# Kernel optimization log

Hardware: AMD Instinct MI355X
Metric: run time of the kernel (lower is better)

Reference implementation:

```python
import jax, jax.numpy as jnp
import numpy as np

V, D, H, B, LK, LQ, PAD = 10000, 300, 512, 16, 64, 64, 0


def _lstm(x, Wih, Whh, b, h0, c0):
    # x: [B,T,D]; Wih: [4G,D]; Whh: [4G,G]; b: [4G] (b_ih+b_hh); torch gate order i,f,g,o
    xg = jnp.einsum('btd,gd->btg', x, Wih) + b
    def step(hc, xt):
        h, c = hc
        g = xt + h @ Whh.T
        i, f, gg, o = jnp.split(g, 4, axis=-1)
        c = jax.nn.sigmoid(f) * c + jax.nn.sigmoid(i) * jnp.tanh(gg)
        h = jax.nn.sigmoid(o) * jnp.tanh(c)
        return (h, c), h
    (hT, cT), hs = jax.lax.scan(step, (h0, c0), jnp.swapaxes(xg, 0, 1))
    return jnp.swapaxes(hs, 0, 1), hT, cT


def setup_inputs() -> dict:
    key = jax.random.key(0)
    ks = jax.random.split(key, 24)
    n = lambda k, s: (jax.random.normal(k, s, jnp.float32) * 0.05)
    return {
        'source': jax.random.randint(ks[0], (B, LK), 0, V),
        'prev_outputs': jax.random.randint(ks[1], (B, LQ), 0, V),
        'emb': n(ks[2], (V, D)),
        'enc_f_Wih': n(ks[3], (4 * H, D)), 'enc_f_Whh': n(ks[4], (4 * H, H)), 'enc_f_b': n(ks[5], (4 * H,)),
        'enc_b_Wih': n(ks[6], (4 * H, D)), 'enc_b_Whh': n(ks[7], (4 * H, H)), 'enc_b_b': n(ks[8], (4 * H,)),
        'dec_Wih': n(ks[9], (8 * H, D)), 'dec_Whh': n(ks[10], (8 * H, 2 * H)), 'dec_b': n(ks[11], (8 * H,)),
        'k_W': n(ks[12], (2 * H, 2 * H)), 'k_b': n(ks[13], (2 * H,)),
        'v_W': n(ks[14], (2 * H, 2 * H)), 'v_b': n(ks[15], (2 * H,)),
        'fc1_W': n(ks[16], (2 * H, 4 * H)), 'fc1_b': n(ks[17], (2 * H,)),
        'fc2_W': n(ks[18], (V, 2 * H)), 'fc2_b': n(ks[19], (V,)),
    }


def reference(source, prev_outputs, emb, enc_f_Wih, enc_f_Whh, enc_f_b,
              enc_b_Wih, enc_b_Whh, enc_b_b, dec_Wih, dec_Whh, dec_b,
              k_W, k_b, v_W, v_b, fc1_W, fc1_b, fc2_W, fc2_b):
    bsz = source.shape[0]
    xs = emb[source]  # [B,LK,300]
    z = jnp.zeros((bsz, H), xs.dtype)
    out_f, hf, cf = _lstm(xs, enc_f_Wih, enc_f_Whh, enc_f_b, z, z)
    out_b, hb, cb = _lstm(xs[:, ::-1], enc_b_Wih, enc_b_Whh, enc_b_b, z, z)
    enc_out = jnp.concatenate([out_f, out_b[:, ::-1]], axis=-1)  # [B,LK,1024]
    # self.change: interleave fwd/bwd channels -> [B,1024]
    h0 = jnp.stack([hf, hb], axis=-1).reshape(bsz, 2 * H)
    c0 = jnp.stack([cf, cb], axis=-1).reshape(bsz, 2 * H)
    Q, _, _ = _lstm(emb[prev_outputs], dec_Wih, dec_Whh, dec_b, h0, c0)  # [B,LQ,1024]
    K = enc_out @ k_W.T + k_b
    Vv = enc_out @ v_W.T + v_b
    M = jnp.einsum('bqc,bkc->bqk', Q, K)
    mask = (source == PAD)[:, None, :]
    M = jnp.where(mask, -jnp.inf, M)
    A = jax.nn.softmax(M, axis=2)
    ctx = jnp.einsum('bqk,bkc->bqc', A, Vv)  # == (A[...,None]*V[:,None]).sum(2)
    x = jnp.tanh(jnp.concatenate([ctx, Q], axis=-1) @ fc1_W.T + fc1_b)  # dropout=identity (eval)
    return x @ fc2_W.T + fc2_b
```

## Files before the change

kernel.cpp:

```cpp
#include <hip/hip_runtime.h>
#include <cmath>

#define BB   16
#define LKK  64
#define LQQ  64
#define DD   300
#define HH   512
#define H2   1024
#define G4   2048
#define G8   4096
#define VV   10000

__device__ __forceinline__ float sigmoidf_(float x) { return 1.f / (1.f + expf(-x)); }

typedef __attribute__((ext_vector_type(4))) float    f4_;
typedef __attribute__((ext_vector_type(4))) unsigned u4_;

__device__ __forceinline__ void st_sc(float* p, float v) {
    __hip_atomic_store(p, v, __ATOMIC_RELAXED, __HIP_MEMORY_SCOPE_AGENT);
}

__device__ __forceinline__ f4_ ld4_sc(const float* p) {
    f4_ r;
    asm volatile("global_load_dwordx4 %0, %1, off sc0 sc1" : "=v"(r) : "v"(p));
    return r;
}
__device__ __forceinline__ u4_ ld4u_sc(const unsigned* p) {
    u4_ r;
    asm volatile("global_load_dwordx4 %0, %1, off sc0 sc1" : "=v"(r) : "v"(p));
    return r;
}
__device__ __forceinline__ void wait_vm0() {
    asm volatile("s_waitcnt vmcnt(0)" ::: "memory");
    __builtin_amdgcn_sched_barrier(0);
}

__device__ __forceinline__ void gbar2(unsigned* flags, int wg, unsigned target) {
    asm volatile("s_waitcnt vmcnt(0)" ::: "memory");
    if (threadIdx.x == 0)
        __hip_atomic_store(&flags[wg], target, __ATOMIC_RELAXED, __HIP_MEMORY_SCOPE_AGENT);
    if (threadIdx.x < 64) {
        for (;;) {
            u4_ f = ld4u_sc(flags + (threadIdx.x << 2));
            wait_vm0();
            unsigned m0 = f[0] < f[1] ? f[0] : f[1];
            unsigned m1 = f[2] < f[3] ? f[2] : f[3];
            unsigned mn = m0 < m1 ? m0 : m1;
            if (__all((int)(mn >= target))) break;
            __builtin_amdgcn_s_sleep(1);
        }
    }
    __syncthreads();
}

__global__ void rev_idx_kernel(const int* __restrict__ src, int* __restrict__ rev,
                               unsigned* __restrict__ bars) {
    int tid = blockIdx.x * blockDim.x + threadIdx.x;
    if (tid < 512) bars[tid] = 0u;
    if (tid < BB * LKK) {
        int b = tid / LKK, t = tid % LKK;
        rev[tid] = src[b * LKK + (LKK - 1 - t)];
    }
}

typedef __attribute__((ext_vector_type(8))) short bfrag8;
typedef __attribute__((ext_vector_type(4))) float facc4;

__device__ __forceinline__ unsigned short f2bf(float x) {
    unsigned u = __float_as_uint(x);
    unsigned r = (u + 0x7fffu + ((u >> 16) & 1u)) >> 16;
    return (unsigned short)r;
}

#define ASTR 40

__device__ __forceinline__ void gemm_core(
        short* __restrict__ Ah, short* __restrict__ Al,
        short* __restrict__ Bh, short* __restrict__ Bl,
        const float* __restrict__ A, const int* __restrict__ gidx, int lda,
        const float* __restrict__ Bw, int ldb,
        const float* __restrict__ bias,
        float* __restrict__ C, int ldc,
        int N, int K, int act, int m0, int n0) {
    int tid = threadIdx.x;
    int lane = tid & 63, w = tid >> 6;
    int wr = w >> 1, wc = w & 1;
    int fr = lane & 15, fg = lane >> 4;

    int sr = tid >> 1, sc = (tid & 1) << 4;
    long abase = gidx ? (long)gidx[m0 + sr] * lda : (long)(m0 + sr) * lda;
    int gn = n0 + sr;
    bool bval = gn < N;
    long bbase = (long)gn * ldb;

    facc4 acc[4][4] = {};

    for (int k0 = 0; k0 < K; k0 += 32) {
        {
            float v[16];
            if (k0 + sc + 16 <= K) {
                const float* ap = A + abase + k0 + sc;
                float4 t0 = *(const float4*)(ap + 0);
                float4 t1 = *(const float4*)(ap + 4);
                float4 t2 = *(const float4*)(ap + 8);
                float4 t3 = *(const float4*)(ap + 12);
                v[0]=t0.x; v[1]=t0.y; v[2]=t0.z;  v[3]=t0.w;
                v[4]=t1.x; v[5]=t1.y; v[6]=t1.z;  v[7]=t1.w;
                v[8]=t2.x; v[9]=t2.y; v[10]=t2.z; v[11]=t2.w;
                v[12]=t3.x; v[13]=t3.y; v[14]=t3.z; v[15]=t3.w;
            } else {
#pragma unroll
                for (int c = 0; c < 16; c++) {
                    int k = k0 + sc + c;
                    v[c] = (k < K) ? A[abase + k] : 0.f;
                }
            }
            bfrag8 h0, h1, l0, l1;
#pragma unroll
            for (int c = 0; c < 8; c++) {
                unsigned short hb = f2bf(v[c]);
                float hf = __uint_as_float(((unsigned)hb) << 16);
                h0[c] = (short)hb; l0[c] = (short)f2bf(v[c] - hf);
            }
#pragma unroll
            for (int c = 0; c < 8; c++) {
                unsigned short hb = f2bf(v[8 + c]);
                float hf = __uint_as_float(((unsigned)hb) << 16);
                h1[c] = (short)hb; l1[c] = (short)f2bf(v[8 + c] - hf);
            }
            *(bfrag8*)&Ah[sr * ASTR + sc]     = h0;
            *(bfrag8*)&Ah[sr * ASTR + sc + 8] = h1;
            *(bfrag8*)&Al[sr * ASTR + sc]     = l0;
            *(bfrag8*)&Al[sr * ASTR + sc + 8] = l1;
        }
        {
            float v[16];
            if (bval && (k0 + sc + 16 <= K)) {
                const float* bp = Bw + bbase + k0 + sc;
                float4 t0 = *(const float4*)(bp + 0);
                float4 t1 = *(const float4*)(bp + 4);
                float4 t2 = *(const float4*)(bp + 8);
                float4 t3 = *(const float4*)(bp + 12);
                v[0]=t0.x; v[1]=t0.y; v[2]=t0.z;  v[3]=t0.w;
                v[4]=t1.x; v[5]=t1.y; v[6]=t1.z;  v[7]=t1.w;
                v[8]=t2.x; v[9]=t2.y; v[10]=t2.z; v[11]=t2.w;
                v[12]=t3.x; v[13]=t3.y; v[14]=t3.z; v[15]=t3.w;
            } else {
#pragma unroll
                for (int c = 0; c < 16; c++) {
                    int k = k0 + sc + c;
                    v[c] = (bval && k < K) ? Bw[bbase + k] : 0.f;
                }
            }
            bfrag8 h0, h1, l0, l1;
#pragma unroll
            for (int c = 0; c < 8; c++) {
                unsigned short hb = f2bf(v[c]);
                float hf = __uint_as_float(((unsigned)hb) << 16);
                h0[c] = (short)hb; l0[c] = (short)f2bf(v[c] - hf);
            }
#pragma unroll
            for (int c = 0; c < 8; c++) {
                unsigned short hb = f2bf(v[8 + c]);
                float hf = __uint_as_float(((unsigned)hb) << 16);
                h1[c] = (short)hb; l1[c] = (short)f2bf(v[8 + c] - hf);
            }
            *(bfrag8*)&Bh[sr * ASTR + sc]     = h0;
            *(bfrag8*)&Bh[sr * ASTR + sc + 8] = h1;
            *(bfrag8*)&Bl[sr * ASTR + sc]     = l0;
            *(bfrag8*)&Bl[sr * ASTR + sc + 8] = l1;
        }
        __syncthreads();

        bfrag8 ah[4], al[4], bh[4], bl[4];
#pragma unroll
        for (int i = 0; i < 4; i++) {
            int ar = wr * 64 + i * 16 + fr;
            ah[i] = *(const bfrag8*)&Ah[ar * ASTR + fg * 8];
            al[i] = *(const bfrag8*)&Al[ar * ASTR + fg * 8];
            int br = wc * 64 + i * 16 + fr;
            bh[i] = *(const bfrag8*)&Bh[br * ASTR + fg * 8];
            bl[i] = *(const bfrag8*)&Bl[br * ASTR + fg * 8];
        }
#pragma unroll
        for (int i = 0; i < 4; i++)
#pragma unroll
            for (int j = 0; j < 4; j++) {
                acc[i][j] = __builtin_amdgcn_mfma_f32_16x16x32_bf16(ah[i], bh[j], acc[i][j], 0, 0, 0);
                acc[i][j] = __builtin_amdgcn_mfma_f32_16x16x32_bf16(ah[i], bl[j], acc[i][j], 0, 0, 0);
                acc[i][j] = __builtin_amdgcn_mfma_f32_16x16x32_bf16(al[i], bh[j], acc[i][j], 0, 0, 0);
            }
        __syncthreads();
    }

#pragma unroll
    for (int i = 0; i < 4; i++) {
        int row = m0 + wr * 64 + i * 16 + fg * 4;
#pragma unroll
        for (int j = 0; j < 4; j++) {
            int col = n0 + wc * 64 + j * 16 + fr;
            if (col < N) {
                float bz = bias[col];
#pragma unroll
                for (int q = 0; q < 4; q++) {
                    float vv = acc[i][j][q] + bz;
                    if (act == 1) vv = tanhf(vv);
                    C[(long)(row + q) * ldc + col] = vv;
                }
            }
        }
    }
}

__global__ __launch_bounds__(256)
void gemm_mfma128(const float* __restrict__ A, const int* __restrict__ gidx, int lda,
                  const float* __restrict__ Bw, int ldb,
                  const float* __restrict__ bias,
                  float* __restrict__ C, int ldc,
                  int N, int K, int act) {
    __shared__ __align__(16) short Ah[128 * ASTR];
    __shared__ __align__(16) short Al[128 * ASTR];
    __shared__ __align__(16) short Bh[128 * ASTR];
    __shared__ __align__(16) short Bl[128 * ASTR];
    gemm_core(Ah, Al, Bh, Bl, A, gidx, lda, Bw, ldb, bias, C, ldc, N, K, act,
              blockIdx.x * 128, blockIdx.y * 128);
}

__global__ __launch_bounds__(256)
void gemm_kv(const float* __restrict__ enc_out,
             const float* __restrict__ kW, const float* __restrict__ kb,
             const float* __restrict__ vW, const float* __restrict__ vb,
             float* __restrict__ Kbuf, float* __restrict__ Vbuf) {
    __shared__ __align__(16) short Ah[128 * ASTR];
    __shared__ __align__(16) short Al[128 * ASTR];
    __shared__ __align__(16) short Bh[128 * ASTR];
    __shared__ __align__(16) short Bl[128 * ASTR];
    int ny = blockIdx.y;
    if (ny < 8)
        gemm_core(Ah, Al, Bh, Bl, enc_out, nullptr, H2, kW, H2, kb, Kbuf, H2,
                  H2, H2, 0, blockIdx.x * 128, ny * 128);
    else
        gemm_core(Ah, Al, Bh, Bl, enc_out, nullptr, H2, vW, H2, vb, Vbuf, H2,
                  H2, H2, 0, blockIdx.x * 128, (ny - 8) * 128);
}

__global__ __launch_bounds__(256)
void gemm_xg(const float* __restrict__ emb,
             const int* __restrict__ src, const int* __restrict__ rev,
             const int* __restrict__ prev,
             const float* __restrict__ Wf, const float* __restrict__ bf,
             const float* __restrict__ Wb, const float* __restrict__ bb,
             const float* __restrict__ Wd, const float* __restrict__ bd,
             float* __restrict__ xf, float* __restrict__ xb,
             float* __restrict__ xd) {
    __shared__ __align__(16) short Ah[128 * ASTR];
    __shared__ __align__(16) short Al[128 * ASTR];
    __shared__ __align__(16) short Bh[128 * ASTR];
    __shared__ __align__(16) short Bl[128 * ASTR];
    int ny = blockIdx.y;
    if (ny < 16)
        gemm_core(Ah, Al, Bh, Bl, emb, src, DD, Wf, DD, bf, xf, G4,
                  G4, DD, 0, blockIdx.x * 128, ny * 128);
    else if (ny < 32)
        gemm_core(Ah, Al, Bh, Bl, emb, rev, DD, Wb, DD, bb, xb, G4,
                  G4, DD, 0, blockIdx.x * 128, (ny - 16) * 128);
    else
        gemm_core(Ah, Al, Bh, Bl, emb, prev, DD, Wd, DD, bd, xd, G8,
                  G8, DD, 0, blockIdx.x * 128, (ny - 32) * 128);
}

__global__ __launch_bounds__(256, 1)
void enc_recur(const float* __restrict__ xg_f, const float* __restrict__ xg_b,
               const float* __restrict__ Wf, const float* __restrict__ Wb,
               float* __restrict__ hglob, float* __restrict__ enc_out,
               float* __restrict__ encc, unsigned* __restrict__ flags) {
    __shared__ float hs[HH * 16];
    __shared__ float red[256 * 33];
    __shared__ float g256[256];
    int wg  = blockIdx.x;
    int dir = wg >> 7;
    int j0  = (wg & 127) * 4;
    int tid = threadIdx.x;
    int ks   = tid & 31;
    int tile = tid >> 5;
    int bh   = tile >> 2;
    int gate = tile & 3;
    int sw   = (ks >> 2) & 3;
    const float* W  = dir ? Wb : Wf;
    const float* xg = dir ? xg_b : xg_f;

    float wreg[4][16];
#pragma unroll
    for (int jn = 0; jn < 4; jn++) {
        const float* wrow = W + (long)(gate * HH + j0 + jn) * HH;
#pragma unroll
        for (int j = 0; j < 16; j++) wreg[jn][j] = wrow[ks + 32 * j];
    }

    int ub = tid & 15, ujj = tid >> 4;
    int xb = tid >> 4, xgate = (tid >> 2) & 3, xjn = tid & 3;
    float creg = 0.f;
    float4* hsv = (float4*)hs;

    for (int t = 0; t < LKK; t++) {
        if (t == 0) {
            for (int i = tid; i < HH * 16; i += 256) hs[i] = 0.f;
        } else {
            const float* hg = hglob + (long)((dir << 1) | (t & 1)) * (HH * 16);
            f4_ vv[8];
#pragma unroll
            for (int u = 0; u < 8; u++) vv[u] = ld4_sc(hg + tid * 4 + u * 1024);
            wait_vm0();
#pragma unroll
            for (int u = 0; u < 8; u++) {
                int e = tid * 4 + u * 1024;
                int jj = e >> 4, b0 = e & 15;
                *(f4_*)&hs[(jj << 4) + ((((b0 >> 2) ^ ((jj >> 2) & 3))) << 2)] = vv[u];
            }
        }
        float xval = xg[(long)(xb * LKK + t) * G4 + xgate * HH + j0 + xjn];
        __syncthreads();

        float acc[8][4];
#pragma unroll
        for (int i = 0; i < 8; i++)
#pragma unroll
            for (int jn = 0; jn < 4; jn++) acc[i][jn] = 0.f;
#pragma unroll
        for (int j = 0; j < 16; j++) {
            int k = ks + 32 * j;
            float4 h0 = hsv[k * 4 + ((bh * 2 + 0) ^ sw)];
            float4 h1 = hsv[k * 4 + ((bh * 2 + 1) ^ sw)];
#pragma unroll
            for (int jn = 0; jn < 4; jn++) {
                float w = wreg[jn][j];
                acc[0][jn] += h0.x * w; acc[1][jn] += h0.y * w;
                acc[2][jn] += h0.z * w; acc[3][jn] += h0.w * w;
                acc[4][jn] += h1.x * w; acc[5][jn] += h1.y * w;
                acc[6][jn] += h1.z * w; acc[7][jn] += h1.w * w;
            }
        }
#pragma unroll
        for (int i = 0; i < 8; i++)
#pragma unroll
            for (int jn = 0; jn < 4; jn++)
                red[((bh * 8 + i) * 16 + gate * 4 + jn) * 33 + ks] = acc[i][jn];
        __syncthreads();
        {
            const float* row = red + tid * 33;
            float s0 = 0.f, s1 = 0.f, s2 = 0.f, s3 = 0.f;
#pragma unroll
            for (int u = 0; u < 8; u++) {
                s0 += row[u * 4 + 0]; s1 += row[u * 4 + 1];
                s2 += row[u * 4 + 2]; s3 += row[u * 4 + 3];
            }
            g256[tid] = ((s0 + s1) + (s2 + s3)) + xval;
        }
        __syncthreads();

        if (tid < 64) {
            int j = j0 + ujj;
            float gi = g256[ub * 16 + 0  + ujj];
            float gf = g256[ub * 16 + 4  + ujj];
            float gg = g256[ub * 16 + 8  + ujj];
            float go = g256[ub * 16 + 12 + ujj];
            float cv = sigmoidf_(gf) * creg + sigmoidf_(gi) * tanhf(gg);
            creg = cv;
            float hv = sigmoidf_(go) * tanhf(cv);
            st_sc(&hglob[(long)((dir << 1) | ((t + 1) & 1)) * (HH * 16) + j * 16 + ub], hv);
            int kpos = dir ? (LKK - 1 - t) : t;
            enc_out[(long)(ub * LKK + kpos) * H2 + dir * HH + j] = hv;
            if (t == LKK - 1) encc[(dir * BB + ub) * HH + j] = creg;
        }
        if (t < LKK - 1) gbar2(flags, wg, (unsigned)(t + 1));
    }
}

__global__ __launch_bounds__(256, 1)
void dec_recur(const float* __restrict__ xg_d, const float* __restrict__ Wd,
               const float* __restrict__ enc_out, const float* __restrict__ encc,
               float* __restrict__ hglob, float* __restrict__ Qout,
               unsigned* __restrict__ flags) {
    __shared__ float hs[HH * 16];
    __shared__ float red[256 * 33];
    __shared__ float g256[256];
    int wg  = blockIdx.x;
    int j0  = wg * 4;
    int tid = threadIdx.x;
    int ks   = tid & 31;
    int tile = tid >> 5;
    int bh   = tile >> 2;
    int gate = tile & 3;
    int sw   = (ks >> 2) & 3;

    float wreg[4][32];
#pragma unroll
    for (int jn = 0; jn < 4; jn++) {
        const float* wrow = Wd + (long)(gate * H2 + j0 + jn) * H2;
#pragma unroll
        for (int j = 0; j < 32; j++) wreg[jn][j] = wrow[ks + 32 * j];
    }

    int ub = tid & 15, ujj = tid >> 4;
    int xb = tid >> 4, xgate = (tid >> 2) & 3, xjn = tid & 3;
    float creg = 0.f;
    if (tid < 64) {
        int j = j0 + ujj;
        creg = ((j & 1) == 0) ? encc[ub * HH + (j >> 1)]
                              : encc[(BB + ub) * HH + (j >> 1)];
    }
    float4* hsv = (float4*)hs;

    for (int t = 0; t < LQQ; t++) {
        float xval = xg_d[(long)(xb * LQQ + t) * G8 + xgate * H2 + j0 + xjn];
        float acc[8][4];
#pragma unroll
        for (int i = 0; i < 8; i++)
#pragma unroll
            for (int jn = 0; jn < 4; jn++) acc[i][jn] = 0.f;

        auto do_fma = [&](int half) {
#pragma unroll
            for (int jj2 = 0; jj2 < 16; jj2++) {
                int j = half * 16 + jj2;
                int kl = ks + 32 * jj2;
                float4 h0 = hsv[kl * 4 + ((bh * 2 + 0) ^ sw)];
                float4 h1 = hsv[kl * 4 + ((bh * 2 + 1) ^ sw)];
#pragma unroll
                for (int jn = 0; jn < 4; jn++) {
                    float w = wreg[jn][j];
                    acc[0][jn] += h0.x * w; acc[1][jn] += h0.y * w;
                    acc[2][jn] += h0.z * w; acc[3][jn] += h0.w * w;
                    acc[4][jn] += h1.x * w; acc[5][jn] += h1.y * w;
                    acc[6][jn] += h1.z * w; acc[7][jn] += h1.w * w;
                }
            }
        };

        if (t == 0) {
            for (int half = 0; half < 2; half++) {
                for (int e = tid; e < HH * 16; e += 256) {
                    int kl = e >> 4, b = e & 15;
                    int k = half * HH + kl;
                    float hv = ((k & 1) == 0)
                        ? enc_out[(long)(b * LKK + (LKK - 1)) * H2 + (k >> 1)]
                        : enc_out[(long)(b * LKK) * H2 + HH + (k >> 1)];
                    hs[(kl << 4) + ((((b >> 2) ^ ((kl >> 2) & 3))) << 2) + (b & 3)] = hv;
                }
                __syncthreads();
                do_fma(half);
                __syncthreads();
            }
        } else {
            const float* hgA = hglob + (long)(t & 1) * (H2 * 16);
            f4_ vvA[8], vvB[8];
#pragma unroll
            for (int u = 0; u < 8; u++) vvA[u] = ld4_sc(hgA + tid * 4 + u * 1024);
            wait_vm0();
#pragma unroll
            for (int u = 0; u < 8; u++) {
                int e = tid * 4 + u * 1024;
                int kl = e >> 4, b0 = e & 15;
                *(f4_*)&hs[(kl << 4) + ((((b0 >> 2) ^ ((kl >> 2) & 3))) << 2)] = vvA[u];
            }
#pragma unroll
            for (int u = 0; u < 8; u++) vvB[u] = ld4_sc(hgA + (HH * 16) + tid * 4 + u * 1024);
            __syncthreads();
            do_fma(0);
            __syncthreads();
            wait_vm0();
#pragma unroll
            for (int u = 0; u < 8; u++) {
                int e = tid * 4 + u * 1024;
                int kl = e >> 4, b0 = e & 15;
                *(f4_*)&hs[(kl << 4) + ((((b0 >> 2) ^ ((kl >> 2) & 3))) << 2)] = vvB[u];
            }
            __syncthreads();
            do_fma(1);
        }

#pragma unroll
        for (int i = 0; i < 8; i++)
#pragma unroll
            for (int jn = 0; jn < 4; jn++)
                red[((bh * 8 + i) * 16 + gate * 4 + jn) * 33 + ks] = acc[i][jn];
        __syncthreads();
        {
            const float* row = red + tid * 33;
            float s0 = 0.f, s1 = 0.f, s2 = 0.f, s3 = 0.f;
#pragma unroll
            for (int u = 0; u < 8; u++) {
                s0 += row[u * 4 + 0]; s1 += row[u * 4 + 1];
                s2 += row[u * 4 + 2]; s3 += row[u * 4 + 3];
            }
            g256[tid] = ((s0 + s1) + (s2 + s3)) + xval;
        }
        __syncthreads();

        if (tid < 64) {
            int j = j0 + ujj;
            float gi = g256[ub * 16 + 0  + ujj];
            float gf = g256[ub * 16 + 4  + ujj];
            float gg = g256[ub * 16 + 8  + ujj];
            float go = g256[ub * 16 + 12 + ujj];
            float cv = sigmoidf_(gf) * creg + sigmoidf_(gi) * tanhf(gg);
            creg = cv;
            float hv = sigmoidf_(go) * tanhf(cv);
            st_sc(&hglob[(long)((t + 1) & 1) * (H2 * 16) + j * 16 + ub], hv);
            Qout[(long)(ub * LQQ + t) * H2 + j] = hv;
        }
        if (t < LQQ - 1) gbar2(flags, wg, (unsigned)(t + 1));
    }
}

__global__ __launch_bounds__(256)
void attention_kernel(const float* __restrict__ Qm, const float* __restrict__ Km,
                      const float* __restrict__ Vm, const int* __restrict__ source,
                      float* __restrict__ concatBuf) {
    int b = blockIdx.x >> 6;
    int q = blockIdx.x & 63;
    int tid = threadIdx.x;
    __shared__ float qrow[H2];
    __shared__ float part[LKK][4];
    __shared__ float aw[LKK];

    for (int i = tid; i < H2; i += 256) qrow[i] = Qm[(long)(b * LQQ + q) * H2 + i];
    __syncthreads();

    int k = tid >> 2, p = tid & 3;
    {
        const float* krow = Km + (long)(b * LKK + k) * H2 + p * 256;
        const float* qp = qrow + p * 256;
        float s = 0.f;
#pragma unroll 4
        for (int i = 0; i < 256; i++) s += qp[i] * krow[i];
        part[k][p] = s;
    }
    __syncthreads();
    if (tid < 64) {
        float sc = part[tid][0] + part[tid][1] + part[tid][2] + part[tid][3];
        bool masked = (source[b * LKK + tid] == 0);
        float m = masked ? -INFINITY : sc;
#pragma unroll
        for (int o = 32; o >= 1; o >>= 1) m = fmaxf(m, __shfl_xor(m, o, 64));
        float e = masked ? 0.f : expf(sc - m);
        float sum = e;
#pragma unroll
        for (int o = 32; o >= 1; o >>= 1) sum += __shfl_xor(sum, o, 64);
        aw[tid] = e / sum;
    }
    __syncthreads();

    for (int c = tid; c < H2; c += 256) {
        float acc = 0.f;
#pragma unroll 8
        for (int kk = 0; kk < LKK; kk++) acc += aw[kk] * Vm[(long)(b * LKK + kk) * H2 + c];
        long row = (long)(b * LQQ + q) * (2 * H2);
        concatBuf[row + c] = acc;
        concatBuf[row + H2 + c] = qrow[c];
    }
}

extern "C" void kernel_launch(void* const* d_in, const int* in_sizes, int n_in,
                              void* d_out, int out_size, void* d_ws, size_t ws_size,
                              hipStream_t stream) {
    const int*   src       = (const int*)  d_in[0];
    const int*   prev      = (const int*)  d_in[1];
    const float* emb       = (const float*)d_in[2];
    const float* enc_f_Wih = (const float*)d_in[3];
    const float* enc_f_Whh = (const float*)d_in[4];
    const float* enc_f_b   = (const float*)d_in[5];
    const float* enc_b_Wih = (const float*)d_in[6];
    const float* enc_b_Whh = (const float*)d_in[7];
    const float* enc_b_b   = (const float*)d_in[8];
    const float* dec_Wih   = (const float*)d_in[9];
    const float* dec_Whh   = (const float*)d_in[10];
    const float* dec_b     = (const float*)d_in[11];
    const float* k_W  = (const float*)d_in[12];
    const float* k_b  = (const float*)d_in[13];
    const float* v_W  = (const float*)d_in[14];
    const float* v_b  = (const float*)d_in[15];
    const float* fc1_W = (const float*)d_in[16];
    const float* fc1_b = (const float*)d_in[17];
    const float* fc2_W = (const float*)d_in[18];
    const float* fc2_b = (const float*)d_in[19];
    float* out = (float*)d_out;

    float* p = (float*)d_ws;
    float* xg_f    = p; p += (long)BB * LKK * G4;
    float* xg_b    = p; p += (long)BB * LKK * G4;
    float* xg_d    = p; p += (long)BB * LQQ * G8;
    float* enc_out = p; p += (long)BB * LKK * H2;
    float* encc    = p; p += 2L * BB * HH;
    float* hg_enc  = p; p += 2L * 2 * HH * 16;
    float* hg_dec  = p; p += 2L * H2 * 16;
    float* Qbuf    = p; p += (long)BB * LQQ * H2;
    float* Kbuf    = p; p += (long)BB * LKK * H2;
    float* Vbuf    = p; p += (long)BB * LKK * H2;
    float* concatB = p; p += (long)BB * LQQ * 2 * H2;
    float* fc1out  = p; p += (long)BB * LQQ * H2;
    int*   rev     = (int*)p; p += (BB * LKK);
    unsigned* bars = (unsigned*)p; p += 512;

    rev_idx_kernel<<<4, 256, 0, stream>>>(src, rev, bars);

    gemm_xg<<<dim3(8, 64), 256, 0, stream>>>(emb, src, rev, prev,
                                             enc_f_Wih, enc_f_b,
                                             enc_b_Wih, enc_b_b,
                                             dec_Wih, dec_b,
                                             xg_f, xg_b, xg_d);

    enc_recur<<<dim3(256), dim3(256), 0, stream>>>(xg_f, xg_b, enc_f_Whh, enc_b_Whh,
                                                   hg_enc, enc_out, encc, bars);

    gemm_kv<<<dim3(8, 16), 256, 0, stream>>>(enc_out, k_W, k_b, v_W, v_b, Kbuf, Vbuf);

    dec_recur<<<dim3(256), dim3(256), 0, stream>>>(xg_d, dec_Whh, enc_out, encc,
                                                   hg_dec, Qbuf, bars + 256);

    attention_kernel<<<BB * LQQ, 256, 0, stream>>>(Qbuf, Kbuf, Vbuf, src, concatB);

    gemm_mfma128<<<dim3(8, 8), 256, 0, stream>>>(concatB, nullptr, 2 * H2, fc1_W, 2 * H2,
                                                 fc1_b, fc1out, H2, H2, 2 * H2, 1);

    gemm_mfma128<<<dim3(8, (VV + 127) / 128), 256, 0, stream>>>(fc1out, nullptr, H2, fc2_W, H2,
                                                                fc2_b, out, VV, VV, H2, 0);
}
```

Baseline: 1.607 ms.

## Overlap hidden-state loads with FMA and defer output stores past grid barrier

The encoder recurrence now splits the hidden-state staging into two halves: it waits only for the first half of the global loads, runs the first half of the FMAs, then stages the rest. The decoder issues both halves of its global loads up front instead of serialising them. In both kernels the enc_out/Qout stores move off the critical path before the grid barrier; they go into a shared buffer and are written by a different wavefront after the barrier. This trades an extra __syncthreads and shared traffic for shorter per-step latency in the serial recurrence.

After: 1.592 ms. No clear change (-0.9%).

```diff
diff --git a/kernel.cpp b/kernel.cpp
--- a/kernel.cpp
+++ b/kernel.cpp
@@ -277,6 +277,7 @@
     __shared__ float hs[HH * 16];
     __shared__ float red[256 * 33];
     __shared__ float g256[256];
+    __shared__ float hout[64];
     int wg  = blockIdx.x;
     int dir = wg >> 7;
     int j0  = (wg & 127) * 4;
@@ -303,43 +304,61 @@
     float4* hsv = (float4*)hs;
 
     for (int t = 0; t < LKK; t++) {
+        float acc[8][4];
+#pragma unroll
+        for (int i = 0; i < 8; i++)
+#pragma unroll
+            for (int jn = 0; jn < 4; jn++) acc[i][jn] = 0.f;
+
+        auto do_fma = [&](int jlo, int jhi) {
+#pragma unroll
+            for (int j = jlo; j < jhi; j++) {
+                int k = ks + 32 * j;
+                float4 h0 = hsv[k * 4 + ((bh * 2 + 0) ^ sw)];
+                float4 h1 = hsv[k * 4 + ((bh * 2 + 1) ^ sw)];
+#pragma unroll
+                for (int jn = 0; jn < 4; jn++) {
+                    float w = wreg[jn][j];
+                    acc[0][jn] += h0.x * w; acc[1][jn] += h0.y * w;
+                    acc[2][jn] += h0.z * w; acc[3][jn] += h0.w * w;
+                    acc[4][jn] += h1.x * w; acc[5][jn] += h1.y * w;
+                    acc[6][jn] += h1.z * w; acc[7][jn] += h1.w * w;
+                }
+            }
+        };
+
+        float xval = xg[(long)(xb * LKK + t) * G4 + xgate * HH + j0 + xjn];
+
         if (t == 0) {
             for (int i = tid; i < HH * 16; i += 256) hs[i] = 0.f;
+            __syncthreads();
+            do_fma(0, 16);
         } else {
             const float* hg = hglob + (long)((dir << 1) | (t & 1)) * (HH * 16);
             f4_ vv[8];
 #pragma unroll
             for (int u = 0; u < 8; u++) vv[u] = ld4_sc(hg + tid * 4 + u * 1024);
-            wait_vm0();
-#pragma unroll
-            for (int u = 0; u < 8; u++) {
+            asm volatile("s_waitcnt vmcnt(4)" ::: "memory");
+            __builtin_amdgcn_sched_barrier(0);
+#pragma unroll
+            for (int u = 0; u < 4; u++) {
                 int e = tid * 4 + u * 1024;
                 int jj = e >> 4, b0 = e & 15;
                 *(f4_*)&hs[(jj << 4) + ((((b0 >> 2) ^ ((jj >> 2) & 3))) << 2)] = vv[u];
             }
-        }
-        float xval = xg[(long)(xb * LKK + t) * G4 + xgate * HH + j0 + xjn];
-        __syncthreads();
-
-        float acc[8][4];
-#pragma unroll
-        for (int i = 0; i < 8; i++)
-#pragma unroll
-            for (int jn = 0; jn < 4; jn++) acc[i][jn] = 0.f;
-#pragma unroll
-        for (int j = 0; j < 16; j++) {
-            int k = ks + 32 * j;
-            float4 h0 = hsv[k * 4 + ((bh * 2 + 0) ^ sw)];
-            float4 h1 = hsv[k * 4 + ((bh * 2 + 1) ^ sw)];
-#pragma unroll
-            for (int jn = 0; jn < 4; jn++) {
-                float w = wreg[jn][j];
-                acc[0][jn] += h0.x * w; acc[1][jn] += h0.y * w;
-                acc[2][jn] += h0.z * w; acc[3][jn] += h0.w * w;
-                acc[4][jn] += h1.x * w; acc[5][jn] += h1.y * w;
-                acc[6][jn] += h1.z * w; acc[7][jn] += h1.w * w;
-            }
-        }
+            __syncthreads();
+            do_fma(0, 8);
+            wait_vm0();
+#pragma unroll
+            for (int u = 4; u < 8; u++) {
+                int e = tid * 4 + u * 1024;
+                int jj = e >> 4, b0 = e & 15;
+                *(f4_*)&hs[(jj << 4) + ((((b0 >> 2) ^ ((jj >> 2) & 3))) << 2)] = vv[u];
+            }
+            __syncthreads();
+            do_fma(8, 16);
+        }
+
 #pragma unroll
         for (int i = 0; i < 8; i++)
 #pragma unroll
@@ -368,11 +387,17 @@
             creg = cv;
             float hv = sigmoidf_(go) * tanhf(cv);
             st_sc(&hglob[(long)((dir << 1) | ((t + 1) & 1)) * (HH * 16) + j * 16 + ub], hv);
+            hout[tid] = hv;
+            if (t == LKK - 1) encc[(dir * BB + ub) * HH + j] = creg;
+        }
+        if (t < LKK - 1) gbar2(flags, wg, (unsigned)(t + 1));
+        else __syncthreads();
+        if (tid >= 64 && tid < 128) {
+            int lt = tid - 64;
+            int j = j0 + (lt >> 4);
             int kpos = dir ? (LKK - 1 - t) : t;
-            enc_out[(long)(ub * LKK + kpos) * H2 + dir * HH + j] = hv;
-            if (t == LKK - 1) encc[(dir * BB + ub) * HH + j] = creg;
-        }
-        if (t < LKK - 1) gbar2(flags, wg, (unsigned)(t + 1));
+            enc_out[(long)((lt & 15) * LKK + kpos) * H2 + dir * HH + j] = hout[lt];
+        }
     }
 }
 
@@ -384,6 +409,7 @@
     __shared__ float hs[HH * 16];
     __shared__ float red[256 * 33];
     __shared__ float g256[256];
+    __shared__ float hout[64];
     int wg  = blockIdx.x;
     int j0  = wg * 4;
     int tid = threadIdx.x;
@@ -456,15 +482,16 @@
             f4_ vvA[8], vvB[8];
 #pragma unroll
             for (int u = 0; u < 8; u++) vvA[u] = ld4_sc(hgA + tid * 4 + u * 1024);
-            wait_vm0();
+#pragma unroll
+            for (int u = 0; u < 8; u++) vvB[u] = ld4_sc(hgA + (HH * 16) + tid * 4 + u * 1024);
+            asm volatile("s_waitcnt vmcnt(8)" ::: "memory");
+            __builtin_amdgcn_sched_barrier(0);
 #pragma unroll
             for (int u = 0; u < 8; u++) {
                 int e = tid * 4 + u * 1024;
                 int kl = e >> 4, b0 = e & 15;
                 *(f4_*)&hs[(kl << 4) + ((((b0 >> 2) ^ ((kl >> 2) & 3))) << 2)] = vvA[u];
             }
-#pragma unroll
-            for (int u = 0; u < 8; u++) vvB[u] = ld4_sc(hgA + (HH * 16) + tid * 4 + u * 1024);
             __syncthreads();
             do_fma(0);
             __syncthreads();
@@ -507,9 +534,15 @@
             creg = cv;
             float hv = sigmoidf_(go) * tanhf(cv);
             st_sc(&hglob[(long)((t + 1) & 1) * (H2 * 16) + j * 16 + ub], hv);
-            Qout[(long)(ub * LQQ + t) * H2 + j] = hv;
+            hout[tid] = hv;
         }
         if (t < LQQ - 1) gbar2(flags, wg, (unsigned)(t + 1));
+        else __syncthreads();
+        if (tid >= 64 && tid < 128) {
+            int lt = tid - 64;
+            int j = j0 + (lt >> 4);
+            Qout[(long)((lt & 15) * LQQ + t) * H2 + j] = hout[lt];
+        }
     }
 }
 
```
